# Kernel optimization log

Measured on AMD Instinct MI355X. Metric: run time of the kernel, lower is better.

Reference implementation:

```python
import jax, jax.numpy as jnp
import numpy as np
from jax import lax

DIM = 192
HEADS = 8
B, H, W = 8, 128, 128


def dwconv3x3(x, w):
    # x: [B,C,H,W], w: [C,1,3,3] depthwise (groups=C)
    return lax.conv_general_dilated(
        x, w, window_strides=(1, 1), padding='SAME',
        feature_group_count=x.shape[1],
        dimension_numbers=('NCHW', 'OIHW', 'NCHW'))


def conv1x1(x, w, b=None):
    # w: [Cout, Cin]
    y = jnp.einsum('oc,bchw->bohw', w, x)
    if b is not None:
        y = y + b[None, :, None, None]
    return y


def setup_inputs() -> dict:
    key = jax.random.key(0)
    ks = jax.random.split(key, 9)
    s = 0.02
    return {
        'x': jax.random.normal(ks[0], (B, DIM, H, W), jnp.float32),
        'w_qkv': jax.random.normal(ks[1], (3 * DIM, DIM), jnp.float32) * s,
        'b_qkv': jnp.zeros((3 * DIM,), jnp.float32),
        'w_dw': jax.random.normal(ks[2], (3 * DIM, 1, 3, 3), jnp.float32) * s,
        'b_dw': jnp.zeros((3 * DIM,), jnp.float32),
        'w_proj': jax.random.normal(ks[3], (DIM, DIM), jnp.float32) * s,
        'b_proj': jnp.zeros((DIM,), jnp.float32),
        'w_pos1': jax.random.normal(ks[4], (DIM, 1, 3, 3), jnp.float32) * s,
        'w_pos2': jax.random.normal(ks[5], (DIM, 1, 3, 3), jnp.float32) * s,
        'temperature': jnp.ones((HEADS, 1, 1), jnp.float32),
    }


def reference(x, w_qkv, b_qkv, w_dw, b_dw, w_proj, b_proj, w_pos1, w_pos2, temperature):
    b, c, h, w = x.shape
    heads = HEADS
    ch = c // heads

    qkv = conv1x1(x, w_qkv, b_qkv)
    qkv = dwconv3x3(qkv, w_dw) + b_dw[None, :, None, None]
    q_inp, k_inp, v_inp = jnp.split(qkv, 3, axis=1)

    def to_heads(t):  # [B,C,H,W] -> [B,heads,ch,HW]
        return t.reshape(b, heads, ch, h * w)

    q = to_heads(q_inp)
    k = to_heads(k_inp)
    v = to_heads(v_inp)

    # L2 normalize over hw (torch F.normalize, eps=1e-12)
    q = q / jnp.maximum(jnp.linalg.norm(q, axis=-1, keepdims=True), 1e-12)
    k = k / jnp.maximum(jnp.linalg.norm(k, axis=-1, keepdims=True), 1e-12)

    attn = jnp.einsum('bhce,bhde->bhcd', q, k) * temperature  # [B,heads,ch,ch]
    attn = jax.nn.softmax(attn, axis=-1)
    out = jnp.einsum('bhcd,bhde->bhce', attn, v)  # [B,heads,ch,HW]
    out = out.reshape(b, c, h, w)

    out = conv1x1(out, w_proj, b_proj)

    pos = dwconv3x3(v_inp, w_pos1)
    pos = jax.nn.gelu(pos, approximate=False)
    pos = dwconv3x3(pos, w_pos2)

    return out + pos
```

## Files before the change

kernel.cpp:

```cpp
#include <hip/hip_runtime.h>
#include <stdint.h>
#include <stddef.h>

#define NB 8
#define CC 192
#define C3 576
#define HGT 128
#define WID 128
#define HW 16384
#define NH 8

typedef short bf16x8 __attribute__((ext_vector_type(8)));
typedef float f32x4 __attribute__((ext_vector_type(4)));

__device__ __forceinline__ unsigned short f2bf(float f) {
  unsigned int u = __float_as_uint(f);
  u += 0x7fffu + ((u >> 16) & 1u);
  return (unsigned short)(u >> 16);
}
__device__ __forceinline__ float bf2f(unsigned short h) {
  return __uint_as_float(((unsigned int)h) << 16);
}
__device__ __forceinline__ unsigned int pk2(float a, float b) {
  return (unsigned int)f2bf(a) | ((unsigned int)f2bf(b) << 16);
}
__device__ __forceinline__ void gl_lds16(const void* g, void* l) {
  __builtin_amdgcn_global_load_lds(
      (const __attribute__((address_space(1))) unsigned int*)(uintptr_t)g,
      (__attribute__((address_space(3))) unsigned int*)(uint32_t)(uintptr_t)l,
      16, 0, 0);
}
__device__ __forceinline__ int xcd_swz(int g, int n) {
  return (g & 7) * (n >> 3) + (g >> 3);
}

__global__ __launch_bounds__(256) void ktrans(const float* __restrict__ x,
                                              unsigned char* __restrict__ xT) {
  __shared__ __align__(16) float lx[192 * 68];
  int wg = xcd_swz(blockIdx.x, gridDim.x);
  int pt = wg & 255, b = wg >> 8;
  int p0 = pt * 64;
  int tid = threadIdx.x;
#pragma unroll
  for (int i = 0; i < 12; ++i) {
    int f = tid + i * 256;
    int ic = f >> 4, q = f & 15;
    float4 v = *(const float4*)(x + ((size_t)(b * CC + ic)) * HW + p0 + q * 4);
    *(float4*)(lx + ic * 68 + q * 4) = v;
  }
  __syncthreads();
#pragma unroll
  for (int i = 0; i < 6; ++i) {
    int f = i * 256 + tid;
    int s = f >> 6, p = f & 63;
    unsigned int wv[4];
#pragma unroll
    for (int j = 0; j < 4; ++j)
      wv[j] = pk2(lx[(s * 8 + 2 * j) * 68 + p], lx[(s * 8 + 2 * j + 1) * 68 + p]);
    uint4 st; st.x = wv[0]; st.y = wv[1]; st.z = wv[2]; st.w = wv[3];
    *(uint4*)(xT + (((size_t)(b * 24 + s)) * HW + p0 + p) * 16) = st;
  }
}

__global__ void kwprep(const float* __restrict__ wq, unsigned char* __restrict__ wb) {
  int f = blockIdx.x * 256 + threadIdx.x;
  if (f >= C3 * 24) return;
  int oc = f / 24, s = f % 24;
  unsigned int wv[4];
#pragma unroll
  for (int j = 0; j < 4; ++j)
    wv[j] = pk2(wq[oc * 192 + s * 8 + 2 * j], wq[oc * 192 + s * 8 + 2 * j + 1]);
  uint4 st; st.x = wv[0]; st.y = wv[1]; st.z = wv[2]; st.w = wv[3];
  *(uint4*)(wb + (size_t)oc * 384 + ((s ^ (oc & 7)) * 16)) = st;
}

__global__ __launch_bounds__(256) void kconv1(const unsigned char* __restrict__ xT,
                                              const unsigned char* __restrict__ wb,
                                              const float* __restrict__ bqkv,
                                              unsigned short* __restrict__ vout,
                                              unsigned char* __restrict__ qkout) {
  __shared__ __align__(16) unsigned char lds[73728];
  int wg = xcd_swz(blockIdx.x, gridDim.x);
  int ot = wg % 9; int rest = wg / 9; int grp = rest & 63; int b = rest >> 6;
  int tid = threadIdx.x;
  const unsigned char* gB = wb + (size_t)ot * 24576;
#pragma unroll
  for (int i = 0; i < 6; ++i)
    gl_lds16(gB + i * 4096 + tid * 16, lds + 49152 + i * 4096 + tid * 16);
  const unsigned char* gA = xT + (size_t)b * 24 * HW * 16;
  int t0 = grp * 4;
  {
    int p0 = t0 * 64;
#pragma unroll
    for (int i = 0; i < 6; ++i) {
      int f = i * 256 + tid;
      gl_lds16(gA + (((size_t)(f >> 6)) * HW + p0 + (f & 63)) * 16, lds + f * 16);
    }
  }
  int lane = tid & 63, w = tid >> 6;
  int l15 = lane & 15, gq = lane >> 4;
  int pw = w * 16;
  float bias[4];
  size_t obase[4];
  int isv[4];
#pragma unroll
  for (int nf = 0; nf < 4; ++nf) {
    int oc = ot * 64 + nf * 16 + l15;
    bias[nf] = bqkv[oc];
    if (oc >= 384) {
      isv[nf] = 1;
      obase[nf] = ((size_t)(b * CC + oc - 384)) * HW * 2;
    } else {
      isv[nf] = 0;
      int part = oc >= 192 ? 1 : 0;
      int cm = oc - part * 192;
      int h = cm / 24, ch = cm % 24;
      obase[nf] = (size_t)(((part * 8 + b) * 8 + h) * 128) * 6144 + ch * 16 + (gq & 1) * 8;
    }
  }
  for (int it = 0; it < 4; ++it) {
    int tile = t0 + it;
    asm volatile("s_waitcnt vmcnt(0)" ::: "memory");
    __syncthreads();
    int nb = it & 1;
    if (it < 3) {
      int p1 = (tile + 1) * 64;
#pragma unroll
      for (int i = 0; i < 6; ++i) {
        int f = i * 256 + tid;
        gl_lds16(gA + (((size_t)(f >> 6)) * HW + p1 + (f & 63)) * 16,
                 lds + ((nb ^ 1) * 24576) + f * 16);
      }
    }
    f32x4 acc[4];
#pragma unroll
    for (int nf = 0; nf < 4; ++nf) acc[nf] = (f32x4){0.f, 0.f, 0.f, 0.f};
#pragma unroll
    for (int kk = 0; kk < 6; ++kk) {
      bf16x8 a = *(const bf16x8*)(lds + nb * 24576 + ((((kk * 4 + gq) << 6) + pw + l15) * 16));
      int cb = kk * 64 + gq * 16;
#pragma unroll
      for (int nf = 0; nf < 4; ++nf) {
        int r = nf * 16 + l15;
        bf16x8 bfr = *(const bf16x8*)(lds + 49152 + r * 384 + (cb ^ ((r & 7) << 4)));
        acc[nf] = __builtin_amdgcn_mfma_f32_16x16x32_bf16(a, bfr, acc[nf], 0, 0, 0);
      }
    }
    int p = tile * 64 + pw + gq * 4;
    int y = p >> 7, x = p & 127;
#pragma unroll
    for (int nf = 0; nf < 4; ++nf) {
      uint2 st;
      st.x = pk2(acc[nf][0] + bias[nf], acc[nf][1] + bias[nf]);
      st.y = pk2(acc[nf][2] + bias[nf], acc[nf][3] + bias[nf]);
      if (isv[nf]) {
        *(uint2*)((unsigned char*)vout + obase[nf] + (size_t)p * 2) = st;
      } else {
        *(uint2*)(qkout + obase[nf] + (size_t)y * 6144 + (x >> 3) * 384) = st;
      }
    }
  }
}

__device__ __forceinline__ void dwoct(const unsigned char* lds, int t, int r0,
                                      int xu, int ch, const float* w, float bias,
                                      float* o) {
#pragma unroll
  for (int j = 0; j < 8; ++j) o[j] = bias;
#pragma unroll
  for (int dy = 0; dy < 3; ++dy) {
    int ub = ((t * 6 + r0 + dy) * 16) * 24 + ch;
    union { bf16x8 v; unsigned short s[8]; } m;
    m.v = *(const bf16x8*)(lds + (size_t)(ub + xu * 24) * 16);
    unsigned short lft = *(const unsigned short*)(lds + (size_t)(ub + (xu > 0 ? xu - 1 : 0) * 24) * 16 + 14);
    unsigned short rgt = *(const unsigned short*)(lds + (size_t)(ub + (xu < 15 ? xu + 1 : 15) * 24) * 16);
    float vwin[10];
    vwin[0] = (xu > 0) ? bf2f(lft) : 0.f;
    vwin[9] = (xu < 15) ? bf2f(rgt) : 0.f;
#pragma unroll
    for (int j = 0; j < 8; ++j) vwin[1 + j] = bf2f(m.s[j]);
#pragma unroll
    for (int j = 0; j < 8; ++j)
      o[j] += vwin[j] * w[dy * 3] + vwin[j + 1] * w[dy * 3 + 1] + vwin[j + 2] * w[dy * 3 + 2];
  }
}

__global__ __launch_bounds__(256) void kqk(const unsigned char* __restrict__ qk,
                                           const float* __restrict__ wdw,
                                           const float* __restrict__ bdw,
                                           float* __restrict__ G,
                                           float* __restrict__ nq,
                                           float* __restrict__ nk) {
  __shared__ __align__(16) unsigned char lds[73728];
  int wg = xcd_swz(blockIdx.x, gridDim.x);
  int band = wg & 31, bh = wg >> 5;
  int h = bh & 7, b = bh >> 3;
  int y0 = band * 4;
  int tid = threadIdx.x;
  if (band == 0 || band == 31) {
#pragma unroll
    for (int i = 0; i < 18; ++i)
      *(uint4*)(lds + (i * 256 + tid) * 16) = (uint4){0, 0, 0, 0};
    __syncthreads();
  }
#pragma unroll
  for (int i = 0; i < 18; ++i) {
    int f = i * 256 + tid;
    int t = f / 2304, rem = f % 2304;
    int r = rem / 384, u = rem % 384;
    int y = y0 - 1 + r;
    if (y >= 0 && y < HGT)
      gl_lds16(qk + ((size_t)(((t * 8 + b) * 8 + h) * 128 + y)) * 6144 + u * 16,
               lds + f * 16);
  }
  asm volatile("s_waitcnt vmcnt(0)" ::: "memory");
  __syncthreads();

  int lane = tid & 63, w = tid >> 6;
  int l15 = lane & 15, gq = lane >> 4;
  int ch0 = l15;
  int ch1 = (l15 < 8) ? 16 + l15 : 23;
  int c0 = h * 24 + ch0, c1 = h * 24 + ch1;
  float wq0[9], wq1[9], wk0[9], wk1[9];
#pragma unroll
  for (int j = 0; j < 9; ++j) {
    wq0[j] = wdw[c0 * 9 + j];        wq1[j] = wdw[c1 * 9 + j];
    wk0[j] = wdw[(192 + c0) * 9 + j]; wk1[j] = wdw[(192 + c1) * 9 + j];
  }
  float bq0 = bdw[c0], bq1 = bdw[c1], bk0 = bdw[192 + c0], bk1 = bdw[192 + c1];

  f32x4 acc[2][2];
#pragma unroll
  for (int ct = 0; ct < 2; ++ct)
#pragma unroll
    for (int dt = 0; dt < 2; ++dt) acc[ct][dt] = (f32x4){0.f, 0.f, 0.f, 0.f};
  float nq0 = 0.f, nq1 = 0.f, nk0 = 0.f, nk1 = 0.f;

#pragma unroll
  for (int j4 = 0; j4 < 4; ++j4) {
    int kt = w * 4 + j4;
    int r0 = kt >> 2;
    int xu = (kt & 3) * 4 + gq;
    union { bf16x8 v; unsigned int u[4]; } fq0, fq1, fk0, fk1;
    {
      float o[8];
      dwoct(lds, 0, r0, xu, ch0, wq0, bq0, o);
#pragma unroll
      for (int j = 0; j < 8; ++j) nq0 += o[j] * o[j];
#pragma unroll
      for (int e = 0; e < 4; ++e) fq0.u[e] = pk2(o[2 * e], o[2 * e + 1]);
    }
    {
      float o[8];
      dwoct(lds, 0, r0, xu, ch1, wq1, bq1, o);
#pragma unroll
      for (int j = 0; j < 8; ++j) nq1 += o[j] * o[j];
#pragma unroll
      for (int e = 0; e < 4; ++e) fq1.u[e] = pk2(o[2 * e], o[2 * e + 1]);
    }
    {
      float o[8];
      dwoct(lds, 1, r0, xu, ch0, wk0, bk0, o);
#pragma unroll
      for (int j = 0; j < 8; ++j) nk0 += o[j] * o[j];
#pragma unroll
      for (int e = 0; e < 4; ++e) fk0.u[e] = pk2(o[2 * e], o[2 * e + 1]);
    }
    {
      float o[8];
      dwoct(lds, 1, r0, xu, ch1, wk1, bk1, o);
#pragma unroll
      for (int j = 0; j < 8; ++j) nk1 += o[j] * o[j];
#pragma unroll
      for (int e = 0; e < 4; ++e) fk1.u[e] = pk2(o[2 * e], o[2 * e + 1]);
    }
    acc[0][0] = __builtin_amdgcn_mfma_f32_16x16x32_bf16(fq0.v, fk0.v, acc[0][0], 0, 0, 0);
    acc[0][1] = __builtin_amdgcn_mfma_f32_16x16x32_bf16(fq0.v, fk1.v, acc[0][1], 0, 0, 0);
    acc[1][0] = __builtin_amdgcn_mfma_f32_16x16x32_bf16(fq1.v, fk0.v, acc[1][0], 0, 0, 0);
    acc[1][1] = __builtin_amdgcn_mfma_f32_16x16x32_bf16(fq1.v, fk1.v, acc[1][1], 0, 0, 0);
  }
  __syncthreads();
  float* gp = (float*)lds;
#pragma unroll
  for (int ct = 0; ct < 2; ++ct)
#pragma unroll
    for (int dt = 0; dt < 2; ++dt)
      *(f32x4*)(gp + (((w * 4 + ct * 2 + dt) * 64) + lane) * 4) = acc[ct][dt];
  nq0 += __shfl_xor(nq0, 16); nq0 += __shfl_xor(nq0, 32);
  nq1 += __shfl_xor(nq1, 16); nq1 += __shfl_xor(nq1, 32);
  nk0 += __shfl_xor(nk0, 16); nk0 += __shfl_xor(nk0, 32);
  nk1 += __shfl_xor(nk1, 16); nk1 += __shfl_xor(nk1, 32);
  int nb24 = (b * NH + h) * 24;
  if (lane < 16) {
    atomicAdd(nq + nb24 + l15, nq0);
    atomicAdd(nk + nb24 + l15, nk0);
  }
  if (lane < 8) {
    atomicAdd(nq + nb24 + 16 + l15, nq1);
    atomicAdd(nk + nb24 + 16 + l15, nk1);
  }
  __syncthreads();
  float* Gb = G + (size_t)(b * NH + h) * 576;
#pragma unroll
  for (int ii = 0; ii < 3; ++ii) {
    int f = ii * 256 + tid;
    if (f < 576) {
      int c = f / 24, d = f % 24;
      int t4 = ((c >> 4) << 1) + (d >> 4);
      int lane16 = (d & 15) + (((c & 15) >> 2) << 4);
      int reg = c & 3;
      float s = 0.f;
#pragma unroll
      for (int w4 = 0; w4 < 4; ++w4)
        s += gp[((w4 * 4 + t4) * 64 + lane16) * 4 + reg];
      atomicAdd(Gb + f, s);
    }
  }
}

__global__ __launch_bounds__(256) void kdwv(const unsigned short* __restrict__ src,
                                            const float* __restrict__ wdw,
                                            const float* __restrict__ bdw,
                                            unsigned char* __restrict__ vT) {
  __shared__ __align__(16) unsigned int smem[8 * 721];
  int wg = xcd_swz(blockIdx.x, gridDim.x);
  int cg = wg % 24, rt = (wg / 24) & 15, b = wg / 384;
  int y0 = rt * 8, chg0 = cg * 8;
  int tid = threadIdx.x;
  for (int i = tid; i < 5768; i += 256) smem[i] = 0;
  __syncthreads();
#pragma unroll
  for (int i = 0; i < 5; ++i) {
    int f = i * 256 + tid;
    int ch = f / 160, rem = f % 160;
    int r = rem >> 4, seg = rem & 15;
    int y = y0 - 1 + r;
    if (y >= 0 && y < HGT) {
      uint4 v = *(const uint4*)(src + ((size_t)(b * CC + chg0 + ch)) * HW + y * WID + seg * 8);
      unsigned int* dp = smem + ch * 721 + r * 72 + 4 + seg * 4;
      dp[0] = v.x; dp[1] = v.y; dp[2] = v.z; dp[3] = v.w;
    }
  }
  __syncthreads();
  int ch = tid >> 5, u = tid & 31;
  int row = u >> 2, xs = (u & 3) * 32;
  int gch = 384 + chg0 + ch;
  float wv[9];
#pragma unroll
  for (int j = 0; j < 9; ++j) wv[j] = wdw[gch * 9 + j];
  float bias = bdw[gch];
  float outv[32];
  const unsigned int* tb = smem + ch * 721;
#pragma unroll
  for (int g = 0; g < 4; ++g) {
    int x0 = xs + g * 8;
    float v[3][12];
#pragma unroll
    for (int dy = 0; dy < 3; ++dy) {
      const unsigned int* rp = tb + (row + dy) * 72 + ((x0 + 6) >> 1);
#pragma unroll
      for (int m = 0; m < 6; ++m) {
        unsigned int w2 = rp[m];
        v[dy][2 * m] = bf2f((unsigned short)(w2 & 0xffff));
        v[dy][2 * m + 1] = bf2f((unsigned short)(w2 >> 16));
      }
    }
#pragma unroll
    for (int j = 0; j < 8; ++j) {
      float a = bias;
#pragma unroll
      for (int dy = 0; dy < 3; ++dy)
#pragma unroll
        for (int dx = 0; dx < 3; ++dx)
          a += v[dy][j + dx + 1] * wv[dy * 3 + dx];
      outv[g * 8 + j] = a;
    }
  }
  __syncthreads();
  unsigned short* vt = (unsigned short*)smem;
#pragma unroll
  for (int g = 0; g < 4; ++g)
#pragma unroll
    for (int j = 0; j < 8; j += 2) {
      int x = xs + g * 8 + j;
      ((unsigned int*)smem)[ch * 512 + row * 64 + (x >> 1)] =
          pk2(outv[g * 8 + j], outv[g * 8 + j + 1]);
    }
  __syncthreads();
#pragma unroll
  for (int i = 0; i < 4; ++i) {
    int f = i * 256 + tid;
    int r = f >> 7, col = f & 127;
    unsigned int wvp[4];
#pragma unroll
    for (int e = 0; e < 4; ++e) {
      unsigned short a = vt[(2 * e) * 1024 + r * 128 + col];
      unsigned short bb = vt[(2 * e + 1) * 1024 + r * 128 + col];
      wvp[e] = (unsigned int)a | ((unsigned int)bb << 16);
    }
    uint4 st; st.x = wvp[0]; st.y = wvp[1]; st.z = wvp[2]; st.w = wvp[3];
    *(uint4*)(vT + (((size_t)(b * 24 + cg)) * HW + (size_t)(y0 + r) * WID + col) * 16) = st;
  }
}

__global__ __launch_bounds__(256) void kattn(const float* __restrict__ G,
                                             const float* __restrict__ nq,
                                             const float* __restrict__ nk,
                                             const float* __restrict__ temp,
                                             const float* __restrict__ wproj,
                                             unsigned char* __restrict__ W2) {
  __shared__ float attn[24][24];
  __shared__ float iq[24], ik[24];
  int bh = blockIdx.x;
  int h = bh & 7, b = bh >> 3;
  int tid = threadIdx.x;
  const float* Gb = G + (size_t)bh * 576;
  if (tid < 24) { float n = sqrtf(nq[bh * 24 + tid]); iq[tid] = 1.f / fmaxf(n, 1e-12f); }
  else if (tid < 48) { float n = sqrtf(nk[bh * 24 + tid - 24]); ik[tid - 24] = 1.f / fmaxf(n, 1e-12f); }
  __syncthreads();
  if (tid < 24) {
    float tmp = temp[h];
    float row[24];
    float mx = -1e30f;
#pragma unroll
    for (int d = 0; d < 24; ++d) {
      row[d] = Gb[tid * 24 + d] * iq[tid] * ik[d] * tmp;
      mx = fmaxf(mx, row[d]);
    }
    float sum = 0.f;
#pragma unroll
    for (int d = 0; d < 24; ++d) { float e = expf(row[d] - mx); row[d] = e; sum += e; }
    float inv = 1.f / sum;
#pragma unroll
    for (int d = 0; d < 24; ++d) attn[tid][d] = row[d] * inv;
  }
  __syncthreads();
  for (int i = 0; i < 18; ++i) {
    int f = tid + i * 256;
    if (f >= 4608) break;
    int oc = f / 24, d = f % 24;
    float s = 0.f;
#pragma unroll
    for (int c = 0; c < 24; ++c) s += wproj[oc * 192 + h * 24 + c] * attn[c][d];
    int gg = h * 24 + d;
    *(unsigned short*)(W2 + ((size_t)b * CC + oc) * 384 + ((gg * 2) ^ ((oc & 7) << 4))) = f2bf(s);
  }
}

__global__ __launch_bounds__(256) void kpos(const unsigned char* __restrict__ vT,
                                            const float* __restrict__ w1,
                                            const float* __restrict__ w2,
                                            unsigned short* __restrict__ pos) {
  __shared__ unsigned int vbuf[8 * 865];
  __shared__ unsigned int d1[8 * 721];
  int wg = xcd_swz(blockIdx.x, gridDim.x);
  int cg = wg % 24, rt = (wg / 24) & 15, b = wg / 384;
  int y0 = rt * 8, g0 = cg * 8;
  int tid = threadIdx.x;
  for (int i = tid; i < 6920; i += 256) vbuf[i] = 0;
  __syncthreads();
#pragma unroll
  for (int i = 0; i < 3; ++i) {
    int f = i * 256 + tid;
    int r = f >> 6, colp = f & 63;
    int y = y0 - 2 + r;
    if (y >= 0 && y < HGT) {
      const unsigned char* base = vT + (((size_t)(b * 24 + cg)) * HW + (size_t)y * WID + colp * 2) * 16;
      uint4 va = *(const uint4*)(base);
      uint4 vb2 = *(const uint4*)(base + 16);
      unsigned int la[4] = {va.x, va.y, va.z, va.w};
      unsigned int lb[4] = {vb2.x, vb2.y, vb2.z, vb2.w};
#pragma unroll
      for (int e = 0; e < 8; ++e) {
        unsigned int a16 = (la[e >> 1] >> ((e & 1) * 16)) & 0xffff;
        unsigned int b16 = (lb[e >> 1] >> ((e & 1) * 16)) & 0xffff;
        vbuf[e * 865 + r * 72 + colp + 4] = a16 | (b16 << 16);
      }
    }
  }
  __syncthreads();
  int ch = tid >> 5, u = tid & 31;
  {
    const float* wp = w1 + (g0 + ch) * 9;
    float wl[9];
#pragma unroll
    for (int j = 0; j < 9; ++j) wl[j] = wp[j];
    int x0 = u * 4;
    for (int rr = 0; rr < 10; ++rr) {
      int y = y0 - 1 + rr;
      unsigned int o0 = 0, o1 = 0;
      if (y >= 0 && y < HGT) {
        float v[3][8];
#pragma unroll
        for (int dy = 0; dy < 3; ++dy) {
          const unsigned int* rp = vbuf + ch * 865 + (rr + dy) * 72 + ((x0 + 6) >> 1);
#pragma unroll
          for (int m = 0; m < 4; ++m) {
            unsigned int w2r = rp[m];
            v[dy][2 * m] = bf2f((unsigned short)(w2r & 0xffff));
            v[dy][2 * m + 1] = bf2f((unsigned short)(w2r >> 16));
          }
        }
        float g4[4];
#pragma unroll
        for (int j = 0; j < 4; ++j) {
          float a = 0.f;
#pragma unroll
          for (int dy = 0; dy < 3; ++dy)
#pragma unroll
            for (int dx = 0; dx < 3; ++dx)
              a += v[dy][j + dx + 1] * wl[dy * 3 + dx];
          g4[j] = 0.5f * a * (1.f + erff(a * 0.70710678118f));
        }
        o0 = pk2(g4[0], g4[1]);
        o1 = pk2(g4[2], g4[3]);
      }
      unsigned int* dp = d1 + ch * 721 + rr * 72 + ((x0 + 8) >> 1);
      dp[0] = o0; dp[1] = o1;
    }
  }
  if (tid < 160) {
    int ech = tid / 20, rem = tid % 20;
    int rr = rem >> 1, side = rem & 1;
    int x = side ? 128 : -1;
    int y = y0 - 1 + rr;
    unsigned short val = 0;
    if (y >= 0 && y < HGT) {
      const float* wp = w1 + (g0 + ech) * 9;
      float a = 0.f;
      const unsigned short* vb16 = (const unsigned short*)(vbuf + ech * 865);
#pragma unroll
      for (int dy = 0; dy < 3; ++dy)
#pragma unroll
        for (int dx = 0; dx < 3; ++dx)
          a += bf2f(vb16[(rr + dy) * 144 + (x + dx + 7)]) * wp[dy * 3 + dx];
      val = f2bf(0.5f * a * (1.f + erff(a * 0.70710678118f)));
    }
    ((unsigned short*)(d1 + ech * 721))[rr * 144 + (x + 8)] = val;
  }
  __syncthreads();
  {
    const float* wp = w2 + (g0 + ch) * 9;
    float wl[9];
#pragma unroll
    for (int j = 0; j < 9; ++j) wl[j] = wp[j];
    int row = u >> 2, xs = (u & 3) * 32;
    size_t rb = ((size_t)(b * CC + g0 + ch)) * HW + (size_t)(y0 + row) * WID;
#pragma unroll
    for (int g = 0; g < 4; ++g) {
      int x0 = xs + g * 8;
      float v[3][12];
#pragma unroll
      for (int dy = 0; dy < 3; ++dy) {
        const unsigned int* rp = d1 + ch * 721 + (row + dy) * 72 + ((x0 + 6) >> 1);
#pragma unroll
        for (int m = 0; m < 6; ++m) {
          unsigned int w2r = rp[m];
          v[dy][2 * m] = bf2f((unsigned short)(w2r & 0xffff));
          v[dy][2 * m + 1] = bf2f((unsigned short)(w2r >> 16));
        }
      }
      uint4 st;
      float o[8];
#pragma unroll
      for (int j = 0; j < 8; ++j) {
        float a = 0.f;
#pragma unroll
        for (int dy = 0; dy < 3; ++dy)
#pragma unroll
          for (int dx = 0; dx < 3; ++dx)
            a += v[dy][j + dx + 1] * wl[dy * 3 + dx];
        o[j] = a;
      }
      st.x = pk2(o[0], o[1]); st.y = pk2(o[2], o[3]);
      st.z = pk2(o[4], o[5]); st.w = pk2(o[6], o[7]);
      *(uint4*)(pos + rb + x0) = st;
    }
  }
}

__global__ __launch_bounds__(256) void kproj(const unsigned char* __restrict__ vT,
                                             const unsigned char* __restrict__ W2,
                                             const float* __restrict__ bproj,
                                             const unsigned short* __restrict__ pos,
                                             float* __restrict__ out) {
  __shared__ __align__(16) unsigned char lds[73728];
  int wg = xcd_swz(blockIdx.x, gridDim.x);
  int ot = wg % 3; int rest = wg / 3; int grp = rest & 63; int b = rest >> 6;
  int tid = threadIdx.x;
  const unsigned char* gB = W2 + ((size_t)(b * 192 + ot * 64)) * 384;
#pragma unroll
  for (int i = 0; i < 6; ++i)
    gl_lds16(gB + i * 4096 + tid * 16, lds + 49152 + i * 4096 + tid * 16);
  const unsigned char* gA = vT + (size_t)b * 24 * HW * 16;
  int t0 = grp * 4;
  {
    int p0 = t0 * 64;
#pragma unroll
    for (int i = 0; i < 6; ++i) {
      int f = i * 256 + tid;
      gl_lds16(gA + (((size_t)(f >> 6)) * HW + p0 + (f & 63)) * 16, lds + f * 16);
    }
  }
  int lane = tid & 63, w = tid >> 6;
  int l15 = lane & 15, gq = lane >> 4;
  int pw = w * 16;
  float bias[4];
  size_t obase[4];
#pragma unroll
  for (int nf = 0; nf < 4; ++nf) {
    int oc = ot * 64 + nf * 16 + l15;
    bias[nf] = bproj[oc];
    obase[nf] = ((size_t)(b * 192 + oc)) * HW;
  }
  for (int it = 0; it < 4; ++it) {
    int tile = t0 + it;
    asm volatile("s_waitcnt vmcnt(0)" ::: "memory");
    __syncthreads();
    int nb = it & 1;
    if (it < 3) {
      int p1 = (tile + 1) * 64;
#pragma unroll
      for (int i = 0; i < 6; ++i) {
        int f = i * 256 + tid;
        gl_lds16(gA + (((size_t)(f >> 6)) * HW + p1 + (f & 63)) * 16,
                 lds + ((nb ^ 1) * 24576) + f * 16);
      }
    }
    f32x4 acc[4];
#pragma unroll
    for (int nf = 0; nf < 4; ++nf) acc[nf] = (f32x4){0.f, 0.f, 0.f, 0.f};
#pragma unroll
    for (int kk = 0; kk < 6; ++kk) {
      bf16x8 a = *(const bf16x8*)(lds + nb * 24576 + ((((kk * 4 + gq) << 6) + pw + l15) * 16));
      int cb = kk * 64 + gq * 16;
#pragma unroll
      for (int nf = 0; nf < 4; ++nf) {
        int r = nf * 16 + l15;
        bf16x8 bfr = *(const bf16x8*)(lds + 49152 + r * 384 + (cb ^ ((r & 7) << 4)));
        acc[nf] = __builtin_amdgcn_mfma_f32_16x16x32_bf16(a, bfr, acc[nf], 0, 0, 0);
      }
    }
    int p = tile * 64 + pw + gq * 4;
#pragma unroll
    for (int nf = 0; nf < 4; ++nf) {
      uint2 pv = *(const uint2*)(pos + obase[nf] + p);
      float4 o;
      o.x = acc[nf][0] + bias[nf] + bf2f((unsigned short)(pv.x & 0xffff));
      o.y = acc[nf][1] + bias[nf] + bf2f((unsigned short)(pv.x >> 16));
      o.z = acc[nf][2] + bias[nf] + bf2f((unsigned short)(pv.y & 0xffff));
      o.w = acc[nf][3] + bias[nf] + bf2f((unsigned short)(pv.y >> 16));
      *(float4*)(out + obase[nf] + p) = o;
    }
  }
}

#define OFF_W   ((size_t)0)
#define OFF_G   ((size_t)221184)
#define OFF_NQ  ((size_t)368640)
#define OFF_NK  ((size_t)374784)
#define OFF_W2  ((size_t)380928)
#define OFF_QK  ((size_t)970752)
#define OFF_V   ((size_t)101634048)
#define OFF_XT  ((size_t)151965696)

extern "C" void kernel_launch(void* const* d_in, const int* in_sizes, int n_in,
                              void* d_out, int out_size, void* d_ws, size_t ws_size,
                              hipStream_t stream) {
  const float* x     = (const float*)d_in[0];
  const float* wqkv  = (const float*)d_in[1];
  const float* bqkv  = (const float*)d_in[2];
  const float* wdw   = (const float*)d_in[3];
  const float* bdw   = (const float*)d_in[4];
  const float* wproj = (const float*)d_in[5];
  const float* bproj = (const float*)d_in[6];
  const float* wpos1 = (const float*)d_in[7];
  const float* wpos2 = (const float*)d_in[8];
  const float* temp  = (const float*)d_in[9];
  unsigned char* ws = (unsigned char*)d_ws;

  hipMemsetAsync(ws + OFF_G, 0, 147456 + 6144 + 6144, stream);
  kwprep<<<54, 256, 0, stream>>>(wqkv, ws + OFF_W);
  ktrans<<<2048, 256, 0, stream>>>(x, ws + OFF_XT);
  kconv1<<<4608, 256, 0, stream>>>(ws + OFF_XT, ws + OFF_W, bqkv,
                                   (unsigned short*)(ws + OFF_V), ws + OFF_QK);
  kqk<<<2048, 256, 0, stream>>>(ws + OFF_QK, wdw, bdw, (float*)(ws + OFF_G),
                                (float*)(ws + OFF_NQ), (float*)(ws + OFF_NK));
  kdwv<<<3072, 256, 0, stream>>>((const unsigned short*)(ws + OFF_V), wdw, bdw,
                                 ws + OFF_XT);
  kattn<<<64, 256, 0, stream>>>((const float*)(ws + OFF_G), (const float*)(ws + OFF_NQ),
                                (const float*)(ws + OFF_NK), temp, wproj, ws + OFF_W2);
  kpos<<<3072, 256, 0, stream>>>(ws + OFF_XT, wpos1, wpos2,
                                 (unsigned short*)(ws + OFF_QK));
  kproj<<<1536, 256, 0, stream>>>(ws + OFF_XT, ws + OFF_W2, bproj,
                                  (const unsigned short*)(ws + OFF_QK), (float*)d_out);
}
```

Baseline: 326.0 us.

## Restructure q/k depthwise conv in kqk with swizzled channel-major layout

The q/k intermediate layout written by kconv1 changes to a per-channel row layout with an XOR swizzle on 16-byte units. kqk now computes the 3x3 depthwise conv with 192 threads, each doing one channel and row-half and reusing a sliding register window of 16 outputs. Results are staged as bf16 fragments in LDS before the MFMA Gram pass. Bands shrink to 2 rows and the grid doubles, aiming to cut redundant LDS loads and scalar unpacking in the conv. The cost is 64 idle threads during the conv phase, larger LDS use (80KB) and more halo reloads from the smaller bands.

```diff
diff --git a/kernel.cpp b/kernel.cpp
--- a/kernel.cpp
+++ b/kernel.cpp
@@ -9,6 +9,7 @@
 #define WID 128
 #define HW 16384
 #define NH 8
+#define QKROW 49152
 
 typedef short bf16x8 __attribute__((ext_vector_type(8)));
 typedef float f32x4 __attribute__((ext_vector_type(4)));
@@ -20,6 +21,12 @@
 }
 __device__ __forceinline__ float bf2f(unsigned short h) {
   return __uint_as_float(((unsigned int)h) << 16);
+}
+__device__ __forceinline__ float bflo(unsigned int v) {
+  return __uint_as_float(v << 16);
+}
+__device__ __forceinline__ float bfhi(unsigned int v) {
+  return __uint_as_float(v & 0xffff0000u);
 }
 __device__ __forceinline__ unsigned int pk2(float a, float b) {
   return (unsigned int)f2bf(a) | ((unsigned int)f2bf(b) << 16);
@@ -102,7 +109,7 @@
   int pw = w * 16;
   float bias[4];
   size_t obase[4];
-  int isv[4];
+  int isv[4], key[4];
 #pragma unroll
   for (int nf = 0; nf < 4; ++nf) {
     int oc = ot * 64 + nf * 16 + l15;
@@ -110,12 +117,13 @@
     if (oc >= 384) {
       isv[nf] = 1;
       obase[nf] = ((size_t)(b * CC + oc - 384)) * HW * 2;
+      key[nf] = 0;
     } else {
       isv[nf] = 0;
       int part = oc >= 192 ? 1 : 0;
       int cm = oc - part * 192;
-      int h = cm / 24, ch = cm % 24;
-      obase[nf] = (size_t)(((part * 8 + b) * 8 + h) * 128) * 6144 + ch * 16 + (gq & 1) * 8;
+      obase[nf] = ((size_t)((part * 8 + b) * 128)) * QKROW + cm * 256;
+      key[nf] = cm & 7;
     }
   }
   for (int it = 0; it < 4; ++it) {
@@ -148,6 +156,7 @@
     }
     int p = tile * 64 + pw + gq * 4;
     int y = p >> 7, x = p & 127;
+    int u = x >> 3, sub = (x & 7) * 2;
 #pragma unroll
     for (int nf = 0; nf < 4; ++nf) {
       uint2 st;
@@ -156,32 +165,9 @@
       if (isv[nf]) {
         *(uint2*)((unsigned char*)vout + obase[nf] + (size_t)p * 2) = st;
       } else {
-        *(uint2*)(qkout + obase[nf] + (size_t)y * 6144 + (x >> 3) * 384) = st;
-      }
-    }
-  }
-}
-
-__device__ __forceinline__ void dwoct(const unsigned char* lds, int t, int r0,
-                                      int xu, int ch, const float* w, float bias,
-                                      float* o) {
-#pragma unroll
-  for (int j = 0; j < 8; ++j) o[j] = bias;
-#pragma unroll
-  for (int dy = 0; dy < 3; ++dy) {
-    int ub = ((t * 6 + r0 + dy) * 16) * 24 + ch;
-    union { bf16x8 v; unsigned short s[8]; } m;
-    m.v = *(const bf16x8*)(lds + (size_t)(ub + xu * 24) * 16);
-    unsigned short lft = *(const unsigned short*)(lds + (size_t)(ub + (xu > 0 ? xu - 1 : 0) * 24) * 16 + 14);
-    unsigned short rgt = *(const unsigned short*)(lds + (size_t)(ub + (xu < 15 ? xu + 1 : 15) * 24) * 16);
-    float vwin[10];
-    vwin[0] = (xu > 0) ? bf2f(lft) : 0.f;
-    vwin[9] = (xu < 15) ? bf2f(rgt) : 0.f;
-#pragma unroll
-    for (int j = 0; j < 8; ++j) vwin[1 + j] = bf2f(m.s[j]);
-#pragma unroll
-    for (int j = 0; j < 8; ++j)
-      o[j] += vwin[j] * w[dy * 3] + vwin[j + 1] * w[dy * 3 + 1] + vwin[j + 2] * w[dy * 3 + 2];
+        *(uint2*)(qkout + obase[nf] + (size_t)y * QKROW + ((u ^ key[nf]) * 16 + sub)) = st;
+      }
+    }
   }
 }
 
@@ -191,114 +177,138 @@
                                            float* __restrict__ G,
                                            float* __restrict__ nq,
                                            float* __restrict__ nk) {
-  __shared__ __align__(16) unsigned char lds[73728];
+  __shared__ __align__(16) unsigned char lds[81920];
+  const int FB = 49152;
   int wg = xcd_swz(blockIdx.x, gridDim.x);
-  int band = wg & 31, bh = wg >> 5;
-  int h = bh & 7, b = bh >> 3;
-  int y0 = band * 4;
+  int band = wg & 63, h = (wg >> 6) & 7, b = wg >> 9;
+  int y0 = band * 2;
   int tid = threadIdx.x;
-  if (band == 0 || band == 31) {
-#pragma unroll
-    for (int i = 0; i < 18; ++i)
-      *(uint4*)(lds + (i * 256 + tid) * 16) = (uint4){0, 0, 0, 0};
-    __syncthreads();
-  }
-#pragma unroll
-  for (int i = 0; i < 18; ++i) {
+#pragma unroll
+  for (int i = 0; i < 12; ++i) {
     int f = i * 256 + tid;
-    int t = f / 2304, rem = f % 2304;
+    int p = f / 1536, rem = f % 1536;
     int r = rem / 384, u = rem % 384;
     int y = y0 - 1 + r;
     if (y >= 0 && y < HGT)
-      gl_lds16(qk + ((size_t)(((t * 8 + b) * 8 + h) * 128 + y)) * 6144 + u * 16,
+      gl_lds16(qk + ((size_t)((p * 8 + b) * 128 + y)) * QKROW + h * 6144 + u * 16,
                lds + f * 16);
+    else
+      *(uint4*)(lds + f * 16) = (uint4){0, 0, 0, 0};
   }
   asm volatile("s_waitcnt vmcnt(0)" ::: "memory");
   __syncthreads();
 
   int lane = tid & 63, w = tid >> 6;
+  if (tid < 192) {
+    int p = tid / 96; int r3m = tid % 96;
+    int ch = r3m >> 2; int row = (r3m >> 1) & 1; int half = r3m & 1;
+    int gc = p * 192 + h * 24 + ch;
+    float wv[9];
+#pragma unroll
+    for (int j = 0; j < 9; ++j) wv[j] = wdw[gc * 9 + j];
+    float bias = bdw[gc];
+    const unsigned char* sbase = lds + p * 24576 + ch * 256;
+    int ckey = ch & 7;
+    unsigned char* fb = lds + FB + p * 16384 + ch * 16;
+    int h8 = half * 8;
+    unsigned int W[3][16];
+#define LOADU(dy_, m_, u_) { \
+    uint4 tt = ((u_) >= 0 && (u_) < 16) \
+        ? *(const uint4*)(sbase + (row + (dy_)) * 6144 + (((u_) ^ ckey) * 16)) \
+        : (uint4){0, 0, 0, 0}; \
+    W[dy_][(m_) * 4 + 0] = tt.x; W[dy_][(m_) * 4 + 1] = tt.y; \
+    W[dy_][(m_) * 4 + 2] = tt.z; W[dy_][(m_) * 4 + 3] = tt.w; }
+#pragma unroll
+    for (int dy = 0; dy < 3; ++dy) {
+#pragma unroll
+      for (int m = 0; m < 4; ++m) { LOADU(dy, m, h8 - 1 + m); }
+    }
+    float nsum = 0.f;
+#pragma unroll
+    for (int c4 = 0; c4 < 4; ++c4) {
+      if (c4 > 0) {
+#pragma unroll
+        for (int dy = 0; dy < 3; ++dy) {
+#pragma unroll
+          for (int e = 0; e < 8; ++e) W[dy][e] = W[dy][8 + e];
+          LOADU(dy, 2, h8 - 1 + c4 * 2 + 2);
+          LOADU(dy, 3, h8 - 1 + c4 * 2 + 3);
+        }
+      }
+      float acc[16];
+#pragma unroll
+      for (int j = 0; j < 16; ++j) acc[j] = bias;
+#pragma unroll
+      for (int dy = 0; dy < 3; ++dy) {
+        float f[18];
+#pragma unroll
+        for (int t2 = 0; t2 < 18; ++t2) {
+          int rel = 7 + t2;
+          unsigned int v = W[dy][rel >> 1];
+          f[t2] = (rel & 1) ? bfhi(v) : bflo(v);
+        }
+#pragma unroll
+        for (int j = 0; j < 16; ++j)
+          acc[j] += f[j] * wv[dy * 3] + f[j + 1] * wv[dy * 3 + 1] + f[j + 2] * wv[dy * 3 + 2];
+      }
+#pragma unroll
+      for (int j = 0; j < 16; ++j) nsum += acc[j] * acc[j];
+      unsigned int pk[8];
+#pragma unroll
+      for (int e = 0; e < 8; ++e) pk[e] = pk2(acc[2 * e], acc[2 * e + 1]);
+      int kt = row * 4 + half * 2 + (c4 >> 1);
+      int gb = (c4 & 1) * 2;
+      uint4 s0; s0.x = pk[0]; s0.y = pk[1]; s0.z = pk[2]; s0.w = pk[3];
+      uint4 s1; s1.x = pk[4]; s1.y = pk[5]; s1.z = pk[6]; s1.w = pk[7];
+      *(uint4*)(fb + kt * 2048 + gb * 512) = s0;
+      *(uint4*)(fb + kt * 2048 + (gb + 1) * 512) = s1;
+    }
+#undef LOADU
+    nsum += __shfl_xor(nsum, 1);
+    nsum += __shfl_xor(nsum, 2);
+    if ((tid & 3) == 0) {
+      float* dst = (p == 0) ? nq : nk;
+      atomicAdd(dst + (b * NH + h) * 24 + ch, nsum);
+    }
+  } else {
+    int t2 = tid - 192;
+#pragma unroll
+    for (int i = 0; i < 8; ++i) {
+      int f = i * 64 + t2;
+      int ch8 = f & 7, gq4 = (f >> 3) & 3, kt8 = (f >> 5) & 7, pp = f >> 8;
+      *(uint4*)(lds + FB + pp * 16384 + kt8 * 2048 + gq4 * 512 + (24 + ch8) * 16) =
+          (uint4){0, 0, 0, 0};
+    }
+  }
+  __syncthreads();
+
   int l15 = lane & 15, gq = lane >> 4;
-  int ch0 = l15;
-  int ch1 = (l15 < 8) ? 16 + l15 : 23;
-  int c0 = h * 24 + ch0, c1 = h * 24 + ch1;
-  float wq0[9], wq1[9], wk0[9], wk1[9];
-#pragma unroll
-  for (int j = 0; j < 9; ++j) {
-    wq0[j] = wdw[c0 * 9 + j];        wq1[j] = wdw[c1 * 9 + j];
-    wk0[j] = wdw[(192 + c0) * 9 + j]; wk1[j] = wdw[(192 + c1) * 9 + j];
-  }
-  float bq0 = bdw[c0], bq1 = bdw[c1], bk0 = bdw[192 + c0], bk1 = bdw[192 + c1];
-
-  f32x4 acc[2][2];
+  f32x4 acc2[2][2];
 #pragma unroll
   for (int ct = 0; ct < 2; ++ct)
 #pragma unroll
-    for (int dt = 0; dt < 2; ++dt) acc[ct][dt] = (f32x4){0.f, 0.f, 0.f, 0.f};
-  float nq0 = 0.f, nq1 = 0.f, nk0 = 0.f, nk1 = 0.f;
-
-#pragma unroll
-  for (int j4 = 0; j4 < 4; ++j4) {
-    int kt = w * 4 + j4;
-    int r0 = kt >> 2;
-    int xu = (kt & 3) * 4 + gq;
-    union { bf16x8 v; unsigned int u[4]; } fq0, fq1, fk0, fk1;
-    {
-      float o[8];
-      dwoct(lds, 0, r0, xu, ch0, wq0, bq0, o);
-#pragma unroll
-      for (int j = 0; j < 8; ++j) nq0 += o[j] * o[j];
-#pragma unroll
-      for (int e = 0; e < 4; ++e) fq0.u[e] = pk2(o[2 * e], o[2 * e + 1]);
-    }
-    {
-      float o[8];
-      dwoct(lds, 0, r0, xu, ch1, wq1, bq1, o);
-#pragma unroll
-      for (int j = 0; j < 8; ++j) nq1 += o[j] * o[j];
-#pragma unroll
-      for (int e = 0; e < 4; ++e) fq1.u[e] = pk2(o[2 * e], o[2 * e + 1]);
-    }
-    {
-      float o[8];
-      dwoct(lds, 1, r0, xu, ch0, wk0, bk0, o);
-#pragma unroll
-      for (int j = 0; j < 8; ++j) nk0 += o[j] * o[j];
-#pragma unroll
-      for (int e = 0; e < 4; ++e) fk0.u[e] = pk2(o[2 * e], o[2 * e + 1]);
-    }
-    {
-      float o[8];
-      dwoct(lds, 1, r0, xu, ch1, wk1, bk1, o);
-#pragma unroll
-      for (int j = 0; j < 8; ++j) nk1 += o[j] * o[j];
-#pragma unroll
-      for (int e = 0; e < 4; ++e) fk1.u[e] = pk2(o[2 * e], o[2 * e + 1]);
-    }
-    acc[0][0] = __builtin_amdgcn_mfma_f32_16x16x32_bf16(fq0.v, fk0.v, acc[0][0], 0, 0, 0);
-    acc[0][1] = __builtin_amdgcn_mfma_f32_16x16x32_bf16(fq0.v, fk1.v, acc[0][1], 0, 0, 0);
-    acc[1][0] = __builtin_amdgcn_mfma_f32_16x16x32_bf16(fq1.v, fk0.v, acc[1][0], 0, 0, 0);
-    acc[1][1] = __builtin_amdgcn_mfma_f32_16x16x32_bf16(fq1.v, fk1.v, acc[1][1], 0, 0, 0);
-  }
-  __syncthreads();
+    for (int dt = 0; dt < 2; ++dt) acc2[ct][dt] = (f32x4){0.f, 0.f, 0.f, 0.f};
+#pragma unroll
+  for (int t2 = 0; t2 < 2; ++t2) {
+    int kt = w * 2 + t2;
+    bf16x8 aq[2], bk[2];
+#pragma unroll
+    for (int ct = 0; ct < 2; ++ct) {
+      aq[ct] = *(const bf16x8*)(lds + FB + kt * 2048 + gq * 512 + (ct * 16 + l15) * 16);
+      bk[ct] = *(const bf16x8*)(lds + FB + 16384 + kt * 2048 + gq * 512 + (ct * 16 + l15) * 16);
+    }
+#pragma unroll
+    for (int ct = 0; ct < 2; ++ct)
+#pragma unroll
+      for (int dt = 0; dt < 2; ++dt)
+        acc2[ct][dt] = __builtin_amdgcn_mfma_f32_16x16x32_bf16(aq[ct], bk[dt], acc2[ct][dt], 0, 0, 0);
+  }
   float* gp = (float*)lds;
 #pragma unroll
   for (int ct = 0; ct < 2; ++ct)
 #pragma unroll
     for (int dt = 0; dt < 2; ++dt)
-      *(f32x4*)(gp + (((w * 4 + ct * 2 + dt) * 64) + lane) * 4) = acc[ct][dt];
-  nq0 += __shfl_xor(nq0, 16); nq0 += __shfl_xor(nq0, 32);
-  nq1 += __shfl_xor(nq1, 16); nq1 += __shfl_xor(nq1, 32);
-  nk0 += __shfl_xor(nk0, 16); nk0 += __shfl_xor(nk0, 32);
-  nk1 += __shfl_xor(nk1, 16); nk1 += __shfl_xor(nk1, 32);
-  int nb24 = (b * NH + h) * 24;
-  if (lane < 16) {
-    atomicAdd(nq + nb24 + l15, nq0);
-    atomicAdd(nk + nb24 + l15, nk0);
-  }
-  if (lane < 8) {
-    atomicAdd(nq + nb24 + 16 + l15, nq1);
-    atomicAdd(nk + nb24 + 16 + l15, nk1);
-  }
+      *(f32x4*)(gp + (((w * 4 + ct * 2 + dt) * 64) + lane) * 4) = acc2[ct][dt];
   __syncthreads();
   float* Gb = G + (size_t)(b * NH + h) * 576;
 #pragma unroll
@@ -684,7 +694,7 @@
   ktrans<<<2048, 256, 0, stream>>>(x, ws + OFF_XT);
   kconv1<<<4608, 256, 0, stream>>>(ws + OFF_XT, ws + OFF_W, bqkv,
                                    (unsigned short*)(ws + OFF_V), ws + OFF_QK);
-  kqk<<<2048, 256, 0, stream>>>(ws + OFF_QK, wdw, bdw, (float*)(ws + OFF_G),
+  kqk<<<4096, 256, 0, stream>>>(ws + OFF_QK, wdw, bdw, (float*)(ws + OFF_G),
                                 (float*)(ws + OFF_NQ), (float*)(ws + OFF_NK));
   kdwv<<<3072, 256, 0, stream>>>((const unsigned short*)(ws + OFF_V), wdw, bdw,
                                  ws + OFF_XT);
```

Measured after the change: 329.9 us. Within noise of the previous version (+1.2%).
